# Kernel optimization log

Measured on AMD Instinct MI355X. Metric: run time of the kernel, lower is better.

## Reference

```python
import jax, jax.numpy as jnp
import numpy as np

N_NODES = 50000


def gcn_conv(x, row, col, deg_inv_sqrt, W, b, num_nodes):
    # PyG GCNConv: h = x @ W; out[i] = sum_{(j->i)} norm_ji * h[j] + b
    # norm_ji = deg^{-1/2}[j] * deg^{-1/2}[i], with self-loops already in (row, col).
    h = x @ W  # [N, C_out]
    norm = deg_inv_sqrt[row] * deg_inv_sqrt[col]  # [E+N]
    msgs = h[row] * norm[:, None]  # gather + scale, [E+N, C_out]
    out = jax.ops.segment_sum(msgs, col, num_segments=num_nodes)
    return out + b


def setup_inputs() -> dict:
    key = jax.random.key(0)
    ks = jax.random.split(key, 8)
    n, e = N_NODES, 1600000
    c_in, c_hid, c_out = 128, 64, 32
    x = jax.random.normal(ks[0], (n, c_in), dtype=jnp.float32)
    edge_index = jax.random.randint(ks[1], (2, e), 0, n, dtype=jnp.int64)
    s1 = 1.0 / np.sqrt(c_in)
    s2 = 1.0 / np.sqrt(c_hid)
    W1 = jax.random.uniform(ks[2], (c_in, c_hid), jnp.float32, -s1, s1)
    b1 = jnp.zeros((c_hid,), jnp.float32)
    W2 = jax.random.uniform(ks[3], (c_hid, c_out), jnp.float32, -s2, s2)
    b2 = jnp.zeros((c_out,), jnp.float32)
    W3 = jax.random.uniform(ks[4], (c_hid, c_out), jnp.float32, -s2, s2)
    b3 = jnp.zeros((c_out,), jnp.float32)
    return {"x": x, "edge_index": edge_index, "W1": W1, "b1": b1,
            "W2": W2, "b2": b2, "W3": W3, "b3": b3}


def reference(x, edge_index, W1, b1, W2, b2, W3, b3):
    n = x.shape[0]
    # add self-loops (PyG GCNConv default add_self_loops=True)
    loop = jnp.arange(n, dtype=edge_index.dtype)
    row = jnp.concatenate([edge_index[0], loop])
    col = jnp.concatenate([edge_index[1], loop])
    # symmetric normalization: deg computed over target nodes (unit edge weights)
    deg = jax.ops.segment_sum(jnp.ones_like(col, dtype=x.dtype), col, num_segments=n)
    deg_inv_sqrt = jnp.where(deg > 0, jax.lax.rsqrt(jnp.maximum(deg, 1.0)), 0.0)
    h = jax.nn.relu(gcn_conv(x, row, col, deg_inv_sqrt, W1, b1, n))
    mu = gcn_conv(h, row, col, deg_inv_sqrt, W2, b2, n)
    logvar = gcn_conv(h, row, col, deg_inv_sqrt, W3, b3, n)
    return (mu, logvar)
```

## Files before the change

kernel.cpp:

```cpp
#include <hip/hip_runtime.h>


#define NBMAX 256
#define NT2 256
#define SLOT 128
#define CAPSH 14
#define CAP (1 << CAPSH)

__device__ __forceinline__ ushort f2bf(float x) {
    unsigned u = __float_as_uint(x);
    u = (u + 0x7FFFu + ((u >> 16) & 1u)) >> 16;
    return (ushort)u;
}
__device__ __forceinline__ float bflo(unsigned u) { return __uint_as_float(u << 16); }
__device__ __forceinline__ float bfhi(unsigned u) { return __uint_as_float(u & 0xFFFF0000u); }

__device__ __forceinline__ void acc8(float* a, uint4 x) {
    a[0] += bflo(x.x); a[1] += bfhi(x.x);
    a[2] += bflo(x.y); a[3] += bfhi(x.y);
    a[4] += bflo(x.z); a[5] += bfhi(x.z);
    a[6] += bflo(x.w); a[7] += bfhi(x.w);
}

__device__ __forceinline__ unsigned sc2(unsigned u, float d) {
    return (unsigned)f2bf(d * bflo(u)) | ((unsigned)f2bf(d * bfhi(u)) << 16);
}

__global__ __launch_bounds__(256) void k_front(const int* __restrict__ row,
                                               const int* __restrict__ col,
                                               const float* __restrict__ x,
                                               const float* __restrict__ W1,
                                               int* __restrict__ binbuf,
                                               unsigned char* __restrict__ cnt,
                                               ushort* __restrict__ hs1b,
                                               int n, int e, int chunk) {
    __shared__ __align__(16) unsigned char smem[40960];
    int t = threadIdx.x;
    if (blockIdx.x < NT2) {
        int* lh = (int*)smem;
        int tile = blockIdx.x;
        int t0 = tile * chunk;
        int t1 = t0 + chunk < e ? t0 + chunk : e;
        for (int i = t; i < NBMAX; i += 256) lh[i] = 0;
        __syncthreads();
        for (int i = t0 + t; i < t1; i += 256) {
            int c = col[i];
            int b = c >> 8;
            int pos = atomicAdd(&lh[b], 1);
            if (pos < SLOT)
                binbuf[(((b << 8) + tile) << 7) + pos] = row[i] | ((c & 255) << 16);
        }
        __syncthreads();
        for (int b = t; b < NBMAX; b += 256) {
            int c = lh[b];
            cnt[(tile << 8) + b] = (unsigned char)(c < SLOT ? c : SLOT);
        }
    } else {
        float4 (*w4)[64] = reinterpret_cast<float4(*)[64]>(smem);
        float4 (*xs)[16][8] = reinterpret_cast<float4(*)[16][8]>(smem + 32768);
        for (int i = t; i < 128 * 64; i += 256) {
            int k = i >> 6, c = i & 63;
            ((float*)&w4[k >> 2][c])[k & 3] = W1[i];
        }
        int wid = t >> 6;
        int lane = t & 63;
        int r0 = (blockIdx.x - NT2) * 64 + wid * 16;
        const float4* x4 = (const float4*)x;
        float acc[16];
#pragma unroll
        for (int r = 0; r < 16; ++r) acc[r] = 0.f;
        __syncthreads();
#pragma unroll
        for (int st = 0; st < 4; ++st) {
#pragma unroll
            for (int j = 0; j < 2; ++j) {
                int idx = j * 64 + lane;
                int rr = r0 + (idx >> 3);
                if (rr >= n) rr = n - 1;
                xs[wid][idx >> 3][idx & 7] = x4[(size_t)rr * 32 + st * 8 + (idx & 7)];
            }
#pragma unroll 2
            for (int k4 = 0; k4 < 8; ++k4) {
                float4 wv = w4[st * 8 + k4][lane];
#pragma unroll
                for (int r = 0; r < 16; ++r) {
                    float4 xv = xs[wid][r][k4];
                    acc[r] = fmaf(xv.x, wv.x, acc[r]);
                    acc[r] = fmaf(xv.y, wv.y, acc[r]);
                    acc[r] = fmaf(xv.z, wv.z, acc[r]);
                    acc[r] = fmaf(xv.w, wv.w, acc[r]);
                }
            }
        }
        ushort* hb = hs1b + (size_t)(lane >> 5) * n * 32 + (lane & 31);
#pragma unroll
        for (int r = 0; r < 16; ++r) {
            int rw = r0 + r;
            if (rw < n) hb[(size_t)rw * 32] = f2bf(acc[r]);
        }
    }
}

__global__ __launch_bounds__(256) void k_build(const int* __restrict__ binbuf,
                                               const unsigned char* __restrict__ cnt,
                                               float* __restrict__ dis,
                                               int* __restrict__ rp2,
                                               ushort* __restrict__ csr,
                                               ushort* __restrict__ hs1b, int n) {
    __shared__ int lcnt[256], s[256], cur[256];
    __shared__ float sdis[256];
    int b = blockIdx.x;
    int t = threadIdx.x;
    int myc = cnt[(t << 8) + b];
    int mybase = ((b << 8) + t) << 7;
    lcnt[t] = 0;
    __syncthreads();
    for (int i = 0; i < myc; ++i) {
        int p = binbuf[mybase + i];
        atomicAdd(&lcnt[(p >> 16) & 255], 1);
    }
    __syncthreads();
    int v = lcnt[t];
    s[t] = v;
    __syncthreads();
    for (int off = 1; off < 256; off <<= 1) {
        int u = (t >= off) ? s[t - off] : 0;
        __syncthreads();
        s[t] += u;
        __syncthreads();
    }
    int node0 = b << 8;
    int nloc = n - node0 < 256 ? n - node0 : 256;
    int lo = b << CAPSH;
    if (t < nloc) {
        int beg = lo + s[t] - v;
        rp2[2 * (node0 + t)] = beg;
        rp2[2 * (node0 + t) + 1] = beg + v;
        cur[t] = beg;
        float dv = rsqrtf((float)v + 1.0f);
        dis[node0 + t] = dv;
        sdis[t] = dv;
    }
    __syncthreads();
    for (int i = 0; i < myc; ++i) {
        int p = binbuf[mybase + i];
        int pos = atomicAdd(&cur[(p >> 16) & 255], 1);
        csr[pos] = (ushort)(p & 0xffff);
    }
    uint4* s0 = (uint4*)hs1b + (size_t)node0 * 4;
    uint4* s1 = (uint4*)hs1b + (size_t)n * 4 + (size_t)node0 * 4;
    for (int idx = t; idx < nloc * 4; idx += 256) {
        float dv = sdis[idx >> 2];
        uint4 u0 = s0[idx], u1 = s1[idx];
        u0.x = sc2(u0.x, dv); u0.y = sc2(u0.y, dv);
        u0.z = sc2(u0.z, dv); u0.w = sc2(u0.w, dv);
        u1.x = sc2(u1.x, dv); u1.y = sc2(u1.y, dv);
        u1.z = sc2(u1.z, dv); u1.w = sc2(u1.w, dv);
        s0[idx] = u0;
        s1[idx] = u1;
    }
}

__global__ __launch_bounds__(256) void k_pull1(const int* __restrict__ rp2,
                                               const ushort* __restrict__ csr,
                                               const ushort* __restrict__ hs1b,
                                               const float* __restrict__ dis,
                                               const float* __restrict__ b1,
                                               ushort* __restrict__ hs2b, int n) {
    int xcd = blockIdx.x & 7;
    int sid = xcd >> 2;
    int idx = (blockIdx.x >> 3) * 4 + (xcd & 3);
    int node = idx * 64 + (threadIdx.x >> 2);
    int c4 = threadIdx.x & 3;
    if (node >= n) return;
    size_t slab = (size_t)sid * n * 32;
    const uint4* h4 = (const uint4*)(hs1b + slab);
    int2 be = ((const int2*)rp2)[node];
    float a[8], b[8];
    uint4 v = h4[(size_t)node * 4 + c4];
    a[0] = bflo(v.x); a[1] = bfhi(v.x); a[2] = bflo(v.y); a[3] = bfhi(v.y);
    a[4] = bflo(v.z); a[5] = bfhi(v.z); a[6] = bflo(v.w); a[7] = bfhi(v.w);
#pragma unroll
    for (int j = 0; j < 8; ++j) b[j] = 0.f;
    int k = be.x;
    for (; k + 8 <= be.y; k += 8) {
        uint4 v0 = h4[(size_t)csr[k] * 4 + c4];
        uint4 v1 = h4[(size_t)csr[k + 1] * 4 + c4];
        uint4 v2 = h4[(size_t)csr[k + 2] * 4 + c4];
        uint4 v3 = h4[(size_t)csr[k + 3] * 4 + c4];
        uint4 v4 = h4[(size_t)csr[k + 4] * 4 + c4];
        uint4 v5 = h4[(size_t)csr[k + 5] * 4 + c4];
        uint4 v6 = h4[(size_t)csr[k + 6] * 4 + c4];
        uint4 v7 = h4[(size_t)csr[k + 7] * 4 + c4];
        acc8(a, v0); acc8(b, v1); acc8(a, v2); acc8(b, v3);
        acc8(a, v4); acc8(b, v5); acc8(a, v6); acc8(b, v7);
    }
    if (k + 4 <= be.y) {
        uint4 v0 = h4[(size_t)csr[k] * 4 + c4];
        uint4 v1 = h4[(size_t)csr[k + 1] * 4 + c4];
        uint4 v2 = h4[(size_t)csr[k + 2] * 4 + c4];
        uint4 v3 = h4[(size_t)csr[k + 3] * 4 + c4];
        acc8(a, v0); acc8(b, v1); acc8(a, v2); acc8(b, v3);
        k += 4;
    }
    for (; k < be.y; ++k) acc8(a, h4[(size_t)csr[k] * 4 + c4]);
    float d = dis[node];
    const float* b1s = b1 + sid * 32;
    float4 bb0 = *(const float4*)(b1s + c4 * 8);
    float4 bb1 = *(const float4*)(b1s + c4 * 8 + 4);
    float bj[8] = {bb0.x, bb0.y, bb0.z, bb0.w, bb1.x, bb1.y, bb1.z, bb1.w};
    float o[8];
#pragma unroll
    for (int j = 0; j < 8; ++j) {
        float tt = fmaf(d, a[j] + b[j], bj[j]);
        o[j] = tt > 0.f ? d * tt : 0.f;
    }
    uint4 w;
    w.x = (unsigned)f2bf(o[0]) | ((unsigned)f2bf(o[1]) << 16);
    w.y = (unsigned)f2bf(o[2]) | ((unsigned)f2bf(o[3]) << 16);
    w.z = (unsigned)f2bf(o[4]) | ((unsigned)f2bf(o[5]) << 16);
    w.w = (unsigned)f2bf(o[6]) | ((unsigned)f2bf(o[7]) << 16);
    ((uint4*)(hs2b + slab))[(size_t)node * 4 + c4] = w;
}

__global__ __launch_bounds__(256) void k_pull2(const int* __restrict__ rp2,
                                               const ushort* __restrict__ csr,
                                               const ushort* __restrict__ hs2b,
                                               const float* __restrict__ dis,
                                               float* __restrict__ gagg, int n) {
    int xcd = blockIdx.x & 7;
    int sid = xcd >> 2;
    int idx = (blockIdx.x >> 3) * 4 + (xcd & 3);
    int node = idx * 64 + (threadIdx.x >> 2);
    int c4 = threadIdx.x & 3;
    if (node >= n) return;
    const uint4* h4 = (const uint4*)(hs2b + (size_t)sid * n * 32);
    int2 be = ((const int2*)rp2)[node];
    float a[8], b[8];
    uint4 v = h4[(size_t)node * 4 + c4];
    a[0] = bflo(v.x); a[1] = bfhi(v.x); a[2] = bflo(v.y); a[3] = bfhi(v.y);
    a[4] = bflo(v.z); a[5] = bfhi(v.z); a[6] = bflo(v.w); a[7] = bfhi(v.w);
#pragma unroll
    for (int j = 0; j < 8; ++j) b[j] = 0.f;
    int k = be.x;
    for (; k + 8 <= be.y; k += 8) {
        uint4 v0 = h4[(size_t)csr[k] * 4 + c4];
        uint4 v1 = h4[(size_t)csr[k + 1] * 4 + c4];
        uint4 v2 = h4[(size_t)csr[k + 2] * 4 + c4];
        uint4 v3 = h4[(size_t)csr[k + 3] * 4 + c4];
        uint4 v4 = h4[(size_t)csr[k + 4] * 4 + c4];
        uint4 v5 = h4[(size_t)csr[k + 5] * 4 + c4];
        uint4 v6 = h4[(size_t)csr[k + 6] * 4 + c4];
        uint4 v7 = h4[(size_t)csr[k + 7] * 4 + c4];
        acc8(a, v0); acc8(b, v1); acc8(a, v2); acc8(b, v3);
        acc8(a, v4); acc8(b, v5); acc8(a, v6); acc8(b, v7);
    }
    if (k + 4 <= be.y) {
        uint4 v0 = h4[(size_t)csr[k] * 4 + c4];
        uint4 v1 = h4[(size_t)csr[k + 1] * 4 + c4];
        uint4 v2 = h4[(size_t)csr[k + 2] * 4 + c4];
        uint4 v3 = h4[(size_t)csr[k + 3] * 4 + c4];
        acc8(a, v0); acc8(b, v1); acc8(a, v2); acc8(b, v3);
        k += 4;
    }
    for (; k < be.y; ++k) acc8(a, h4[(size_t)csr[k] * 4 + c4]);
    float d = dis[node];
    float* dst = gagg + (size_t)node * 64 + sid * 32 + c4 * 8;
    *(float4*)dst = make_float4(d * (a[0] + b[0]), d * (a[1] + b[1]),
                                d * (a[2] + b[2]), d * (a[3] + b[3]));
    *(float4*)(dst + 4) = make_float4(d * (a[4] + b[4]), d * (a[5] + b[5]),
                                      d * (a[6] + b[6]), d * (a[7] + b[7]));
}

__global__ __launch_bounds__(256) void k_gemm23(const float* __restrict__ g,
                                                const float* __restrict__ W2,
                                                const float* __restrict__ b2,
                                                const float* __restrict__ W3,
                                                const float* __restrict__ b3,
                                                float* __restrict__ out, int n) {
    __shared__ float ws[2 * 32 * 17 * 4];
    __shared__ float4 gs[4][16 * 16];
    for (int i = threadIdx.x; i < 64 * 32; i += 256) {
        int k = i >> 5, c = i & 31;
        int a = (c * 17 + (k >> 2)) * 4 + (k & 3);
        ws[a] = W2[i];
        ws[2176 + a] = W3[i];
    }
    int wid = threadIdx.x >> 6;
    int lane = threadIdx.x & 63;
    int half = lane >> 5;
    int ch = lane & 31;
    int r0 = blockIdx.x * 64 + wid * 16;
    const float4* g4 = (const float4*)g;
#pragma unroll
    for (int j = 0; j < 4; ++j) {
        int idx = j * 64 + lane;
        int rr = r0 + (idx >> 4);
        if (rr >= n) rr = n - 1;
        gs[wid][idx] = g4[(size_t)rr * 16 + (idx & 15)];
    }
    __syncthreads();
    float acc[16];
#pragma unroll
    for (int r = 0; r < 16; ++r) acc[r] = 0.f;
    const float4* wl = (const float4*)ws;
    const float4* gw = gs[wid];
#pragma unroll 2
    for (int k4 = 0; k4 < 16; ++k4) {
        float4 wv = wl[half * 544 + ch * 17 + k4];
#pragma unroll
        for (int r = 0; r < 16; ++r) {
            float4 gv = gw[r * 16 + k4];
            acc[r] = fmaf(gv.x, wv.x, acc[r]);
            acc[r] = fmaf(gv.y, wv.y, acc[r]);
            acc[r] = fmaf(gv.z, wv.z, acc[r]);
            acc[r] = fmaf(gv.w, wv.w, acc[r]);
        }
    }
    float bb = half ? b3[ch] : b2[ch];
    size_t obase = half ? (size_t)n * 32 : 0;
#pragma unroll
    for (int r = 0; r < 16; ++r) {
        int rw = r0 + r;
        if (rw < n) out[obase + (size_t)rw * 32 + ch] = acc[r] + bb;
    }
}

extern "C" void kernel_launch(void* const* d_in, const int* in_sizes, int n_in,
                              void* d_out, int out_size, void* d_ws, size_t ws_size,
                              hipStream_t stream) {
    const float* x  = (const float*)d_in[0];
    const int*   ei = (const int*)d_in[1];
    const float* W1 = (const float*)d_in[2];
    const float* b1 = (const float*)d_in[3];
    const float* W2 = (const float*)d_in[4];
    const float* b2 = (const float*)d_in[5];
    const float* W3 = (const float*)d_in[6];
    const float* b3 = (const float*)d_in[7];

    int n = in_sizes[0] / 128;
    int e = in_sizes[1] / 2;
    int nb = (n + 255) >> 8;
    const int* row = ei;
    const int* col = ei + e;

    float* fws   = (float*)d_ws;
    float* dis   = fws;
    ushort* hs1b = (ushort*)(fws + n);
    ushort* hs2b = hs1b + (size_t)2 * n * 32;
    int* rp2     = (int*)(hs2b + (size_t)2 * n * 32);
    ushort* csr  = (ushort*)(rp2 + 2 * (size_t)n);
    float* gagg  = (float*)(csr + (size_t)nb * CAP);
    int* binbuf  = (int*)(gagg + (size_t)n * 64);
    unsigned char* cnt = (unsigned char*)(binbuf + (size_t)nb * NT2 * SLOT);
    float* out   = (float*)d_out;

    int chunk = (e + NT2 - 1) / NT2;
    int ntiles = (n + 63) / 64;
    int pg = ntiles;
    int pgrid = 8 * ((pg + 3) / 4);

    dim3 blk(256);
    k_front<<<NT2 + ntiles, blk, 0, stream>>>(row, col, x, W1, binbuf, cnt, hs1b, n, e, chunk);
    k_build<<<nb, blk, 0, stream>>>(binbuf, cnt, dis, rp2, csr, hs1b, n);
    k_pull1<<<pgrid, blk, 0, stream>>>(rp2, csr, hs1b, dis, b1, hs2b, n);
    k_pull2<<<pgrid, blk, 0, stream>>>(rp2, csr, hs2b, dis, gagg, n);
    k_gemm23<<<(n + 63) / 64, blk, 0, stream>>>(gagg, W2, b2, W3, b3, out, n);
}
```

Baseline: 128.1 us.

## Stage W1 per k-slice in smaller LDS and use nontemporal output stores

The GEMM branch of the front kernel no longer copies all of W1 into 32KB of shared memory up front. It loads one 32-row slice per stage with coalesced float4 reads, cutting LDS to 16KB so more blocks can be resident, at the cost of extra barriers per stage. Separately, the outputs written by the pull and GEMM kernels now use nontemporal stores, which avoids polluting the cache with data that is not reread soon.

```diff
diff --git a/kernel.cpp b/kernel.cpp
--- a/kernel.cpp
+++ b/kernel.cpp
@@ -6,6 +6,9 @@
 #define SLOT 128
 #define CAPSH 14
 #define CAP (1 << CAPSH)
+
+typedef unsigned int uint4v __attribute__((ext_vector_type(4)));
+typedef float float4v __attribute__((ext_vector_type(4)));
 
 __device__ __forceinline__ ushort f2bf(float x) {
     unsigned u = __float_as_uint(x);
@@ -34,7 +37,7 @@
                                                unsigned char* __restrict__ cnt,
                                                ushort* __restrict__ hs1b,
                                                int n, int e, int chunk) {
-    __shared__ __align__(16) unsigned char smem[40960];
+    __shared__ __align__(16) unsigned char smem[16384];
     int t = threadIdx.x;
     if (blockIdx.x < NT2) {
         int* lh = (int*)smem;
@@ -56,22 +59,31 @@
             cnt[(tile << 8) + b] = (unsigned char)(c < SLOT ? c : SLOT);
         }
     } else {
-        float4 (*w4)[64] = reinterpret_cast<float4(*)[64]>(smem);
-        float4 (*xs)[16][8] = reinterpret_cast<float4(*)[16][8]>(smem + 32768);
-        for (int i = t; i < 128 * 64; i += 256) {
-            int k = i >> 6, c = i & 63;
-            ((float*)&w4[k >> 2][c])[k & 3] = W1[i];
-        }
+        float4 (*ws)[64] = reinterpret_cast<float4(*)[64]>(smem);
+        float4 (*xs)[16][8] = reinterpret_cast<float4(*)[16][8]>(smem + 8192);
         int wid = t >> 6;
         int lane = t & 63;
         int r0 = (blockIdx.x - NT2) * 64 + wid * 16;
         const float4* x4 = (const float4*)x;
+        const float4* W4g = (const float4*)W1;
         float acc[16];
 #pragma unroll
         for (int r = 0; r < 16; ++r) acc[r] = 0.f;
-        __syncthreads();
 #pragma unroll
         for (int st = 0; st < 4; ++st) {
+            if (st) __syncthreads();
+#pragma unroll
+            for (int j = 0; j < 2; ++j) {
+                int f = j * 256 + t;
+                float4 wv = W4g[st * 512 + f];
+                int klocal = f >> 4;
+                int c0 = (f & 15) * 4;
+                int k4 = klocal >> 2, comp = klocal & 3;
+                ((float*)&ws[k4][c0])[comp]     = wv.x;
+                ((float*)&ws[k4][c0 + 1])[comp] = wv.y;
+                ((float*)&ws[k4][c0 + 2])[comp] = wv.z;
+                ((float*)&ws[k4][c0 + 3])[comp] = wv.w;
+            }
 #pragma unroll
             for (int j = 0; j < 2; ++j) {
                 int idx = j * 64 + lane;
@@ -79,9 +91,10 @@
                 if (rr >= n) rr = n - 1;
                 xs[wid][idx >> 3][idx & 7] = x4[(size_t)rr * 32 + st * 8 + (idx & 7)];
             }
+            __syncthreads();
 #pragma unroll 2
             for (int k4 = 0; k4 < 8; ++k4) {
-                float4 wv = w4[st * 8 + k4][lane];
+                float4 wv = ws[k4][lane];
 #pragma unroll
                 for (int r = 0; r < 16; ++r) {
                     float4 xv = xs[wid][r][k4];
@@ -215,12 +228,12 @@
         float tt = fmaf(d, a[j] + b[j], bj[j]);
         o[j] = tt > 0.f ? d * tt : 0.f;
     }
-    uint4 w;
+    uint4v w;
     w.x = (unsigned)f2bf(o[0]) | ((unsigned)f2bf(o[1]) << 16);
     w.y = (unsigned)f2bf(o[2]) | ((unsigned)f2bf(o[3]) << 16);
     w.z = (unsigned)f2bf(o[4]) | ((unsigned)f2bf(o[5]) << 16);
     w.w = (unsigned)f2bf(o[6]) | ((unsigned)f2bf(o[7]) << 16);
-    ((uint4*)(hs2b + slab))[(size_t)node * 4 + c4] = w;
+    __builtin_nontemporal_store(w, (uint4v*)((uint4*)(hs2b + slab) + (size_t)node * 4 + c4));
 }
 
 __global__ __launch_bounds__(256) void k_pull2(const int* __restrict__ rp2,
@@ -266,10 +279,12 @@
     for (; k < be.y; ++k) acc8(a, h4[(size_t)csr[k] * 4 + c4]);
     float d = dis[node];
     float* dst = gagg + (size_t)node * 64 + sid * 32 + c4 * 8;
-    *(float4*)dst = make_float4(d * (a[0] + b[0]), d * (a[1] + b[1]),
-                                d * (a[2] + b[2]), d * (a[3] + b[3]));
-    *(float4*)(dst + 4) = make_float4(d * (a[4] + b[4]), d * (a[5] + b[5]),
-                                      d * (a[6] + b[6]), d * (a[7] + b[7]));
+    float4v o0 = {d * (a[0] + b[0]), d * (a[1] + b[1]),
+                  d * (a[2] + b[2]), d * (a[3] + b[3])};
+    float4v o1 = {d * (a[4] + b[4]), d * (a[5] + b[5]),
+                  d * (a[6] + b[6]), d * (a[7] + b[7])};
+    __builtin_nontemporal_store(o0, (float4v*)dst);
+    __builtin_nontemporal_store(o1, (float4v*)(dst + 4));
 }
 
 __global__ __launch_bounds__(256) void k_gemm23(const float* __restrict__ g,
@@ -322,7 +337,8 @@
 #pragma unroll
     for (int r = 0; r < 16; ++r) {
         int rw = r0 + r;
-        if (rw < n) out[obase + (size_t)rw * 32 + ch] = acc[r] + bb;
+        if (rw < n)
+            __builtin_nontemporal_store(acc[r] + bb, out + obase + (size_t)rw * 32 + ch);
     }
 }
 
```

Result: faster. 118.3 us (-7.7%).
